# Performance work log

Measured on AMD Instinct MI355X. Metric: run time of the kernel, lower is better.

The kernel has to match this reference:

```python
import jax, jax.numpy as jnp
import numpy as np

B, T, C, H = 8, 2048, 1024, 64

def setup_inputs() -> dict:
    key = jax.random.key(0)
    k0, k1, k2, k3 = jax.random.split(key, 4)
    s = C ** -0.5
    return {
        "x": jax.random.normal(k0, (B, T, C), dtype=jnp.float32),
        "Wq": jax.random.normal(k1, (C, H), dtype=jnp.float32) * s,
        "Wk": jax.random.normal(k2, (C, H), dtype=jnp.float32) * s,
        "Wv": jax.random.normal(k3, (C, H), dtype=jnp.float32) * s,
    }

def reference(x, Wq, Wk, Wv):
    # x: [B,T,C]; Wq/Wk/Wv: [C,H]
    q = jnp.einsum('btc,ch->bth', x, Wq)
    k = jnp.einsum('btc,ch->bth', x, Wk)
    v = jnp.einsum('btc,ch->bth', x, Wv)
    Tn, Cn = x.shape[1], x.shape[2]
    # NOTE: original scales by C**-0.5 (n_embed), not head_size**-0.5
    wei = jnp.einsum('bqh,bkh->bqk', q, k) * (Cn ** -0.5)  # [B,T,T]
    causal = jnp.tril(jnp.ones((Tn, Tn), dtype=bool))
    wei = jnp.where(causal, wei, -jnp.inf)
    wei = jax.nn.softmax(wei, axis=-1)
    # dropout is identity in eval mode
    out = jnp.einsum('bqk,bkh->bqh', wei, v)  # [B,T,H]
    return out
```

## Files before the change

### kernel.cpp

```cpp
#include <hip/hip_runtime.h>
#include <hip/hip_bf16.h>

typedef __attribute__((ext_vector_type(8))) short short8;
typedef __attribute__((ext_vector_type(4))) float f32x4;
typedef __attribute__((ext_vector_type(4))) unsigned short u16x4;
typedef unsigned short u16;

#define Bn 8
#define Tn 2048
#define Cn 1024
#define Hn 64
#define Mrows (Bn * Tn)

__device__ __forceinline__ u16 bfu(float f) {
    __hip_bfloat16 h = __float2bfloat16(f);
    union { __hip_bfloat16 h; u16 u; } c; c.h = h; return c.u;
}

__device__ __forceinline__ short8 cvt8(f32x4 a0, f32x4 a1) {
    short8 r;
    r[0] = (short)bfu(a0[0]); r[1] = (short)bfu(a0[1]);
    r[2] = (short)bfu(a0[2]); r[3] = (short)bfu(a0[3]);
    r[4] = (short)bfu(a1[0]); r[5] = (short)bfu(a1[1]);
    r[6] = (short)bfu(a1[2]); r[7] = (short)bfu(a1[3]);
    return r;
}

__global__ void convert_w3(const float* __restrict__ Wq, const float* __restrict__ Wk,
                           const float* __restrict__ Wv, u16* __restrict__ wtf, float qscale) {
    int widx = blockIdx.x * 256 + threadIdx.x;
    int mat = widx >> 16;
    int rem = widx & 65535;
    int k = rem >> 6, n = rem & 63;
    const float* W = mat == 0 ? Wq : (mat == 1 ? Wk : Wv);
    float s = mat == 0 ? qscale : 1.0f;
    int ct = mat * 4 + (n >> 4);
    int lane = ((k >> 3) & 3) * 16 + (n & 15);
    wtf[(size_t)(ct * 32 + (k >> 5)) * 512 + lane * 8 + (k & 7)] = bfu(W[rem] * s);
}

__global__ __launch_bounds__(512) void qkv_proj(const float* __restrict__ x,
                                                const u16* __restrict__ wtf,
                                                u16* __restrict__ qfl,
                                                u16* __restrict__ kfl,
                                                u16* __restrict__ vfl) {
    __shared__ u16 As[2][32][136];
    const int tid = threadIdx.x;
    const int lane = tid & 63;
    const int wid = tid >> 6;
    const int wm = wid >> 2;
    const int wn = wid & 3;
    const int l15 = lane & 15;
    const int lhi = lane >> 4;
    const int row0 = blockIdx.x * 32;

    const int arow = tid >> 4;
    const int ac0 = (tid & 15) * 8;
    const float* asrc = x + (size_t)(row0 + arow) * Cn + ac0;

    f32x4 acc[3];
    for (int nj = 0; nj < 3; ++nj) acc[nj] = f32x4{0.f, 0.f, 0.f, 0.f};

    f32x4 r0 = *(const f32x4*)(asrc);
    f32x4 r1 = *(const f32x4*)(asrc + 4);
    *(short8*)&As[0][arow][ac0] = cvt8(r0, r1);
    r0 = *(const f32x4*)(asrc + 128);
    r1 = *(const f32x4*)(asrc + 132);
    __syncthreads();

    for (int ks = 0; ks < 8; ++ks) {
        const int cur = ks & 1;
        if (ks < 7) {
            *(short8*)&As[cur ^ 1][arow][ac0] = cvt8(r0, r1);
            if (ks < 6) {
                const float* nsrc = asrc + (size_t)(ks + 2) * 128;
                r0 = *(const f32x4*)(nsrc);
                r1 = *(const f32x4*)(nsrc + 4);
            }
        }
        #pragma unroll
        for (int kc = 0; kc < 4; ++kc) {
            short8 af = *(const short8*)&As[cur][wm * 16 + l15][kc * 32 + lhi * 8];
            #pragma unroll
            for (int nj = 0; nj < 3; ++nj) {
                short8 bf = *(const short8*)(wtf + (size_t)((wn * 3 + nj) * 32 + ks * 4 + kc) * 512 + lane * 8);
                acc[nj] = __builtin_amdgcn_mfma_f32_16x16x32_bf16(af, bf, acc[nj], 0, 0, 0);
            }
        }
        __syncthreads();
    }

    const int growb = row0 + wm * 16 + lhi * 4;
    const int bI = growb >> 11;
    const int tloc = growb & 2047;
    #pragma unroll
    for (int nj = 0; nj < 3; ++nj) {
        const int gcolb = wn * 48 + nj * 16;
        const int matid = gcolb >> 6;
        const int d0 = gcolb & 63;
        if (matid < 2) {
            u16* dst = matid == 0 ? qfl : kfl;
            const int g = tloc >> 4;
            const int lhid = ((d0 & 31) + l15) >> 3;
            const size_t base = ((size_t)(bI * 128 + g) * 2 + (d0 >> 5)) * 512
                                + (size_t)lhid * 128 + (l15 & 7);
            for (int r = 0; r < 4; ++r)
                dst[base + (size_t)(lhi * 4 + r) * 8] = bfu(acc[nj][r]);
        } else {
            const int kt64 = tloc >> 6;
            const int tin = tloc & 63;
            const int kcv = tin >> 5;
            const int lhiv = (tin & 31) >> 3;
            const int e0 = tin & 7;
            const int dt = d0 >> 4;
            u16x4 pk;
            pk[0] = bfu(acc[nj][0]); pk[1] = bfu(acc[nj][1]);
            pk[2] = bfu(acc[nj][2]); pk[3] = bfu(acc[nj][3]);
            *(u16x4*)(vfl + ((size_t)((bI * 32 + kt64) * 4 + dt) * 2 + kcv) * 512
                          + (size_t)(lhiv * 16 + l15) * 8 + e0) = pk;
        }
    }
}

__global__ __launch_bounds__(256) void attn_fwd(const u16* __restrict__ qfl,
                                                const u16* __restrict__ kfl,
                                                const u16* __restrict__ vfl,
                                                float* __restrict__ out) {
    __shared__ float o_lds[4][16][68];
    __shared__ float ml_lds[4][2][16];
    __shared__ u16 pl[4][16][72];
    const int tid = threadIdx.x;
    const int lane = tid & 63;
    const int w = tid >> 6;
    const int l15 = lane & 15, lhi = lane >> 4;
    const int idx = (int)blockIdx.x;
    const int qt = 127 - (idx >> 3);
    const int b = idx & 7;
    const int nkt = (qt >> 2) + 1;
    const int q0 = qt * 16;

    const u16* qb = qfl + (size_t)b * 131072;
    const u16* kb = kfl + (size_t)b * 131072;
    const u16* vb = vfl + (size_t)b * 131072;

    short8 qf[2];
    #pragma unroll
    for (int kc = 0; kc < 2; ++kc)
        qf[kc] = *(const short8*)(qb + ((size_t)(qt * 2 + kc) * 64 + lane) * 8);

    float m = -1e30f, lpart = 0.f;
    f32x4 o[4];
    for (int dt = 0; dt < 4; ++dt) o[dt] = f32x4{0.f, 0.f, 0.f, 0.f};

    for (int kbi = w; kbi < nkt; kbi += 4) {
        const int k0 = kbi * 64;
        short8 kf[2][4], vf[4][2];
        #pragma unroll
        for (int kc = 0; kc < 2; ++kc)
            #pragma unroll
            for (int kt = 0; kt < 4; ++kt)
                kf[kc][kt] = *(const short8*)(kb + ((size_t)((kbi * 4 + kt) * 2 + kc) * 64 + lane) * 8);
        #pragma unroll
        for (int dt = 0; dt < 4; ++dt)
            #pragma unroll
            for (int kc = 0; kc < 2; ++kc)
                vf[dt][kc] = *(const short8*)(vb + ((size_t)((kbi * 4 + dt) * 2 + kc) * 512 + lane * 8));

        f32x4 sacc[4];
        for (int kt = 0; kt < 4; ++kt) sacc[kt] = f32x4{0.f, 0.f, 0.f, 0.f};
        #pragma unroll
        for (int kc = 0; kc < 2; ++kc)
            #pragma unroll
            for (int kt = 0; kt < 4; ++kt)
                sacc[kt] = __builtin_amdgcn_mfma_f32_16x16x32_bf16(kf[kc][kt], qf[kc], sacc[kt], 0, 0, 0);

        if (kbi == nkt - 1) {
            for (int kt = 0; kt < 4; ++kt)
                for (int r = 0; r < 4; ++r) {
                    int kg = k0 + kt * 16 + lhi * 4 + r;
                    if (kg > q0 + l15) sacc[kt][r] = -3.0e38f;
                }
        }
        f32x4 mx0, mx1;
        for (int e = 0; e < 4; ++e) {
            mx0[e] = fmaxf(sacc[0][e], sacc[1][e]);
            mx1[e] = fmaxf(sacc[2][e], sacc[3][e]);
        }
        float tmax = -3.0e38f;
        for (int e = 0; e < 4; ++e) tmax = fmaxf(tmax, fmaxf(mx0[e], mx1[e]));
        tmax = fmaxf(tmax, __shfl_xor(tmax, 16));
        tmax = fmaxf(tmax, __shfl_xor(tmax, 32));
        if (!__all(tmax <= m + 8.0f)) {
            float mnew = fmaxf(m, tmax);
            float corr = exp2f(m - mnew);
            m = mnew;
            lpart *= corr;
            for (int r = 0; r < 4; ++r) {
                float cr = __shfl(corr, lhi * 4 + r);
                for (int dt = 0; dt < 4; ++dt) o[dt][r] *= cr;
            }
        }
        float psum = 0.f;
        for (int kt = 0; kt < 4; ++kt)
            for (int r = 0; r < 4; ++r) {
                float p = exp2f(sacc[kt][r] - m);
                sacc[kt][r] = p;
                psum += p;
            }
        lpart += psum;
        for (int kt = 0; kt < 4; ++kt) {
            u16x4 pk;
            pk[0] = bfu(sacc[kt][0]); pk[1] = bfu(sacc[kt][1]);
            pk[2] = bfu(sacc[kt][2]); pk[3] = bfu(sacc[kt][3]);
            *(u16x4*)&pl[w][l15][kt * 16 + lhi * 4] = pk;
        }
        short8 pf[2];
        #pragma unroll
        for (int kc = 0; kc < 2; ++kc)
            pf[kc] = *(const short8*)&pl[w][l15][kc * 32 + lhi * 8];
        #pragma unroll
        for (int dt = 0; dt < 4; ++dt)
            #pragma unroll
            for (int kc = 0; kc < 2; ++kc)
                o[dt] = __builtin_amdgcn_mfma_f32_16x16x32_bf16(pf[kc], vf[dt][kc], o[dt], 0, 0, 0);
    }
    float lsum = lpart;
    lsum += __shfl_xor(lsum, 16);
    lsum += __shfl_xor(lsum, 32);

    for (int dt = 0; dt < 4; ++dt)
        for (int r = 0; r < 4; ++r)
            o_lds[w][lhi * 4 + r][dt * 16 + l15] = o[dt][r];
    if (lhi == 0) {
        ml_lds[w][0][l15] = m;
        ml_lds[w][1][l15] = lsum;
    }
    __syncthreads();

    float* ob = out + ((size_t)b * Tn + q0) * Hn;
    #pragma unroll
    for (int i = 0; i < 4; ++i) {
        const int e = tid + 256 * i;
        const int row = e >> 6, d = e & 63;
        float M = -3.0e38f;
        #pragma unroll
        for (int ww = 0; ww < 4; ++ww) M = fmaxf(M, ml_lds[ww][0][row]);
        float L = 0.f, acc = 0.f;
        #pragma unroll
        for (int ww = 0; ww < 4; ++ww) {
            float wgt = exp2f(ml_lds[ww][0][row] - M);
            L += ml_lds[ww][1][row] * wgt;
            acc += o_lds[ww][row][d] * wgt;
        }
        ob[(size_t)row * Hn + d] = acc / L;
    }
}

extern "C" void kernel_launch(void* const* d_in, const int* in_sizes, int n_in,
                              void* d_out, int out_size, void* d_ws, size_t ws_size,
                              hipStream_t stream) {
    const float* x = (const float*)d_in[0];
    const float* Wq = (const float*)d_in[1];
    const float* Wk = (const float*)d_in[2];
    const float* Wv = (const float*)d_in[3];
    float* out = (float*)d_out;
    char* ws = (char*)d_ws;

    u16* wtf = (u16*)ws;
    u16* qfl = (u16*)(ws + 196608 * 2);
    u16* kfl = qfl + (size_t)Bn * 131072;
    u16* vfl = kfl + (size_t)Bn * 131072;

    const float qscale = 0.04508422002778011f;
    convert_w3<<<768, 256, 0, stream>>>(Wq, Wk, Wv, wtf, qscale);
    qkv_proj<<<Mrows / 32, 512, 0, stream>>>(x, wtf, qfl, kfl, vfl);
    attn_fwd<<<1024, 256, 0, stream>>>(qfl, kfl, vfl, out);
}
```

Before: 47.65 us.

## Fuse weight convert, QKV projection and attention into one cooperative persistent kernel

Merges the three kernels into one templated kernel and launches it cooperatively with grid-wide syncs between phases, so two kernel launch gaps go away. Blocks loop persistently over tiles and share one LDS union across phases. The projection is retiled to 256 threads per 32-row tile, with each wave computing two M subtiles, and the A-tile double buffering is dropped in favour of a single buffer with two barriers per k-step. If the cooperative launch fails it falls back to three separate launches. Risks are grid-sync cost, lower occupancy, and the attention phase's causal load imbalance now being spread over fewer resident blocks.

Result: slower. 189.1 us (+296.9%).

```diff
diff --git a/kernel.cpp b/kernel.cpp
--- a/kernel.cpp
+++ b/kernel.cpp
@@ -1,5 +1,8 @@
 #include <hip/hip_runtime.h>
 #include <hip/hip_bf16.h>
+#include <hip/hip_cooperative_groups.h>
+
+namespace cg = cooperative_groups;
 
 typedef __attribute__((ext_vector_type(8))) short short8;
 typedef __attribute__((ext_vector_type(4))) float f32x4;
@@ -26,233 +29,244 @@
     return r;
 }
 
-__global__ void convert_w3(const float* __restrict__ Wq, const float* __restrict__ Wk,
-                           const float* __restrict__ Wv, u16* __restrict__ wtf, float qscale) {
-    int widx = blockIdx.x * 256 + threadIdx.x;
-    int mat = widx >> 16;
-    int rem = widx & 65535;
-    int k = rem >> 6, n = rem & 63;
-    const float* W = mat == 0 ? Wq : (mat == 1 ? Wk : Wv);
-    float s = mat == 0 ? qscale : 1.0f;
-    int ct = mat * 4 + (n >> 4);
-    int lane = ((k >> 3) & 3) * 16 + (n & 15);
-    wtf[(size_t)(ct * 32 + (k >> 5)) * 512 + lane * 8 + (k & 7)] = bfu(W[rem] * s);
-}
-
-__global__ __launch_bounds__(512) void qkv_proj(const float* __restrict__ x,
-                                                const u16* __restrict__ wtf,
+template <int PHASE>
+__global__ __launch_bounds__(256, 4) void fused(const float* __restrict__ x,
+                                                const float* __restrict__ Wq,
+                                                const float* __restrict__ Wk,
+                                                const float* __restrict__ Wv,
+                                                u16* __restrict__ wtf,
                                                 u16* __restrict__ qfl,
                                                 u16* __restrict__ kfl,
-                                                u16* __restrict__ vfl) {
-    __shared__ u16 As[2][32][136];
+                                                u16* __restrict__ vfl,
+                                                float* __restrict__ out,
+                                                float qscale) {
+    union Smem {
+        struct { u16 As[32][136]; } q;
+        struct { float o[4][16][68]; float ml[4][2][16]; u16 pl[4][16][72]; } a;
+    };
+    __shared__ Smem sm;
     const int tid = threadIdx.x;
+    const int nb = (int)gridDim.x;
     const int lane = tid & 63;
-    const int wid = tid >> 6;
-    const int wm = wid >> 2;
-    const int wn = wid & 3;
     const int l15 = lane & 15;
     const int lhi = lane >> 4;
-    const int row0 = blockIdx.x * 32;
-
-    const int arow = tid >> 4;
-    const int ac0 = (tid & 15) * 8;
-    const float* asrc = x + (size_t)(row0 + arow) * Cn + ac0;
-
-    f32x4 acc[3];
-    for (int nj = 0; nj < 3; ++nj) acc[nj] = f32x4{0.f, 0.f, 0.f, 0.f};
-
-    f32x4 r0 = *(const f32x4*)(asrc);
-    f32x4 r1 = *(const f32x4*)(asrc + 4);
-    *(short8*)&As[0][arow][ac0] = cvt8(r0, r1);
-    r0 = *(const f32x4*)(asrc + 128);
-    r1 = *(const f32x4*)(asrc + 132);
-    __syncthreads();
-
-    for (int ks = 0; ks < 8; ++ks) {
-        const int cur = ks & 1;
-        if (ks < 7) {
-            *(short8*)&As[cur ^ 1][arow][ac0] = cvt8(r0, r1);
-            if (ks < 6) {
-                const float* nsrc = asrc + (size_t)(ks + 2) * 128;
-                r0 = *(const f32x4*)(nsrc);
-                r1 = *(const f32x4*)(nsrc + 4);
-            }
+
+    if (PHASE == -1 || PHASE == 0) {
+        for (int widx = (int)blockIdx.x * 256 + tid; widx < 196608; widx += nb * 256) {
+            int mat = widx >> 16;
+            int rem = widx & 65535;
+            int k = rem >> 6, n = rem & 63;
+            const float* W = mat == 0 ? Wq : (mat == 1 ? Wk : Wv);
+            float s = mat == 0 ? qscale : 1.0f;
+            int ct = mat * 4 + (n >> 4);
+            int ln = ((k >> 3) & 3) * 16 + (n & 15);
+            wtf[(size_t)(ct * 32 + (k >> 5)) * 512 + ln * 8 + (k & 7)] = bfu(W[rem] * s);
         }
-        #pragma unroll
-        for (int kc = 0; kc < 4; ++kc) {
-            short8 af = *(const short8*)&As[cur][wm * 16 + l15][kc * 32 + lhi * 8];
-            #pragma unroll
-            for (int nj = 0; nj < 3; ++nj) {
-                short8 bf = *(const short8*)(wtf + (size_t)((wn * 3 + nj) * 32 + ks * 4 + kc) * 512 + lane * 8);
-                acc[nj] = __builtin_amdgcn_mfma_f32_16x16x32_bf16(af, bf, acc[nj], 0, 0, 0);
+    }
+    if (PHASE == -1) cg::this_grid().sync();
+
+    if (PHASE == -1 || PHASE == 1) {
+        const int wn = tid >> 6;
+        const int arow = tid >> 3;
+        const int ac0 = (tid & 7) * 16;
+        for (int tile = (int)blockIdx.x; tile < 512; tile += nb) {
+            const int row0 = tile * 32;
+            const float* asrc = x + (size_t)(row0 + arow) * Cn + ac0;
+
+            f32x4 acc[2][3];
+            for (int mt = 0; mt < 2; ++mt)
+                for (int nj = 0; nj < 3; ++nj) acc[mt][nj] = f32x4{0.f, 0.f, 0.f, 0.f};
+
+            f32x4 ra0 = *(const f32x4*)(asrc);
+            f32x4 ra1 = *(const f32x4*)(asrc + 4);
+            f32x4 ra2 = *(const f32x4*)(asrc + 8);
+            f32x4 ra3 = *(const f32x4*)(asrc + 12);
+
+            for (int ks = 0; ks < 8; ++ks) {
+                __syncthreads();
+                *(short8*)&sm.q.As[arow][ac0]     = cvt8(ra0, ra1);
+                *(short8*)&sm.q.As[arow][ac0 + 8] = cvt8(ra2, ra3);
+                __syncthreads();
+                #pragma unroll
+                for (int kc = 0; kc < 4; ++kc) {
+                    short8 af0 = *(const short8*)&sm.q.As[l15][kc * 32 + lhi * 8];
+                    short8 af1 = *(const short8*)&sm.q.As[16 + l15][kc * 32 + lhi * 8];
+                    #pragma unroll
+                    for (int nj = 0; nj < 3; ++nj) {
+                        short8 bf = *(const short8*)(wtf + (size_t)((wn * 3 + nj) * 32 + ks * 4 + kc) * 512 + lane * 8);
+                        acc[0][nj] = __builtin_amdgcn_mfma_f32_16x16x32_bf16(af0, bf, acc[0][nj], 0, 0, 0);
+                        acc[1][nj] = __builtin_amdgcn_mfma_f32_16x16x32_bf16(af1, bf, acc[1][nj], 0, 0, 0);
+                    }
+                }
+                if (ks < 7) {
+                    const float* nsrc = asrc + (size_t)(ks + 1) * 128;
+                    ra0 = *(const f32x4*)(nsrc);
+                    ra1 = *(const f32x4*)(nsrc + 4);
+                    ra2 = *(const f32x4*)(nsrc + 8);
+                    ra3 = *(const f32x4*)(nsrc + 12);
+                }
+            }
+
+            for (int mt = 0; mt < 2; ++mt) {
+                const int growb = row0 + mt * 16 + lhi * 4;
+                const int bI = growb >> 11;
+                const int tloc = growb & 2047;
+                for (int nj = 0; nj < 3; ++nj) {
+                    const int gcolb = wn * 48 + nj * 16;
+                    const int matid = gcolb >> 6;
+                    const int d0 = gcolb & 63;
+                    if (matid < 2) {
+                        u16* dst = matid == 0 ? qfl : kfl;
+                        const int g = tloc >> 4;
+                        const int lhid = ((d0 & 31) + l15) >> 3;
+                        const size_t base = ((size_t)(bI * 128 + g) * 2 + (d0 >> 5)) * 512
+                                            + (size_t)lhid * 128 + (l15 & 7);
+                        for (int r = 0; r < 4; ++r)
+                            dst[base + (size_t)(lhi * 4 + r) * 8] = bfu(acc[mt][nj][r]);
+                    } else {
+                        const int kt64 = tloc >> 6;
+                        const int tin = tloc & 63;
+                        const int kcv = tin >> 5;
+                        const int lhiv = (tin & 31) >> 3;
+                        const int e0 = tin & 7;
+                        const int dt = d0 >> 4;
+                        u16x4 pk;
+                        pk[0] = bfu(acc[mt][nj][0]); pk[1] = bfu(acc[mt][nj][1]);
+                        pk[2] = bfu(acc[mt][nj][2]); pk[3] = bfu(acc[mt][nj][3]);
+                        *(u16x4*)(vfl + ((size_t)((bI * 32 + kt64) * 4 + dt) * 2 + kcv) * 512
+                                      + (size_t)(lhiv * 16 + l15) * 8 + e0) = pk;
+                    }
+                }
             }
         }
-        __syncthreads();
-    }
-
-    const int growb = row0 + wm * 16 + lhi * 4;
-    const int bI = growb >> 11;
-    const int tloc = growb & 2047;
-    #pragma unroll
-    for (int nj = 0; nj < 3; ++nj) {
-        const int gcolb = wn * 48 + nj * 16;
-        const int matid = gcolb >> 6;
-        const int d0 = gcolb & 63;
-        if (matid < 2) {
-            u16* dst = matid == 0 ? qfl : kfl;
-            const int g = tloc >> 4;
-            const int lhid = ((d0 & 31) + l15) >> 3;
-            const size_t base = ((size_t)(bI * 128 + g) * 2 + (d0 >> 5)) * 512
-                                + (size_t)lhid * 128 + (l15 & 7);
-            for (int r = 0; r < 4; ++r)
-                dst[base + (size_t)(lhi * 4 + r) * 8] = bfu(acc[nj][r]);
-        } else {
-            const int kt64 = tloc >> 6;
-            const int tin = tloc & 63;
-            const int kcv = tin >> 5;
-            const int lhiv = (tin & 31) >> 3;
-            const int e0 = tin & 7;
-            const int dt = d0 >> 4;
-            u16x4 pk;
-            pk[0] = bfu(acc[nj][0]); pk[1] = bfu(acc[nj][1]);
-            pk[2] = bfu(acc[nj][2]); pk[3] = bfu(acc[nj][3]);
-            *(u16x4*)(vfl + ((size_t)((bI * 32 + kt64) * 4 + dt) * 2 + kcv) * 512
-                          + (size_t)(lhiv * 16 + l15) * 8 + e0) = pk;
-        }
-    }
-}
-
-__global__ __launch_bounds__(256) void attn_fwd(const u16* __restrict__ qfl,
-                                                const u16* __restrict__ kfl,
-                                                const u16* __restrict__ vfl,
-                                                float* __restrict__ out) {
-    __shared__ float o_lds[4][16][68];
-    __shared__ float ml_lds[4][2][16];
-    __shared__ u16 pl[4][16][72];
-    const int tid = threadIdx.x;
-    const int lane = tid & 63;
-    const int w = tid >> 6;
-    const int l15 = lane & 15, lhi = lane >> 4;
-    const int idx = (int)blockIdx.x;
-    const int qt = 127 - (idx >> 3);
-    const int b = idx & 7;
-    const int nkt = (qt >> 2) + 1;
-    const int q0 = qt * 16;
-
-    const u16* qb = qfl + (size_t)b * 131072;
-    const u16* kb = kfl + (size_t)b * 131072;
-    const u16* vb = vfl + (size_t)b * 131072;
-
-    short8 qf[2];
-    #pragma unroll
-    for (int kc = 0; kc < 2; ++kc)
-        qf[kc] = *(const short8*)(qb + ((size_t)(qt * 2 + kc) * 64 + lane) * 8);
-
-    float m = -1e30f, lpart = 0.f;
-    f32x4 o[4];
-    for (int dt = 0; dt < 4; ++dt) o[dt] = f32x4{0.f, 0.f, 0.f, 0.f};
-
-    for (int kbi = w; kbi < nkt; kbi += 4) {
-        const int k0 = kbi * 64;
-        short8 kf[2][4], vf[4][2];
-        #pragma unroll
-        for (int kc = 0; kc < 2; ++kc)
-            #pragma unroll
-            for (int kt = 0; kt < 4; ++kt)
-                kf[kc][kt] = *(const short8*)(kb + ((size_t)((kbi * 4 + kt) * 2 + kc) * 64 + lane) * 8);
-        #pragma unroll
-        for (int dt = 0; dt < 4; ++dt)
+    }
+    if (PHASE == -1) cg::this_grid().sync();
+
+    if (PHASE == -1 || PHASE == 2) {
+        const int w = tid >> 6;
+        for (int unit = (int)blockIdx.x; unit < 1024; unit += nb) {
+            const int qt = 127 - (unit >> 3);
+            const int b = unit & 7;
+            const int nkt = (qt >> 2) + 1;
+            const int q0 = qt * 16;
+
+            const u16* qb = qfl + (size_t)b * 131072;
+            const u16* kb = kfl + (size_t)b * 131072;
+            const u16* vb = vfl + (size_t)b * 131072;
+
+            short8 qf[2];
             #pragma unroll
             for (int kc = 0; kc < 2; ++kc)
-                vf[dt][kc] = *(const short8*)(vb + ((size_t)((kbi * 4 + dt) * 2 + kc) * 512 + lane * 8));
-
-        f32x4 sacc[4];
-        for (int kt = 0; kt < 4; ++kt) sacc[kt] = f32x4{0.f, 0.f, 0.f, 0.f};
-        #pragma unroll
-        for (int kc = 0; kc < 2; ++kc)
+                qf[kc] = *(const short8*)(qb + ((size_t)(qt * 2 + kc) * 64 + lane) * 8);
+
+            float m = -1e30f, lpart = 0.f;
+            f32x4 o[4];
+            for (int dt = 0; dt < 4; ++dt) o[dt] = f32x4{0.f, 0.f, 0.f, 0.f};
+
+            for (int kbi = w; kbi < nkt; kbi += 4) {
+                const int k0 = kbi * 64;
+                short8 kf[2][4], vf[4][2];
+                #pragma unroll
+                for (int kc = 0; kc < 2; ++kc)
+                    #pragma unroll
+                    for (int kt = 0; kt < 4; ++kt)
+                        kf[kc][kt] = *(const short8*)(kb + ((size_t)((kbi * 4 + kt) * 2 + kc) * 64 + lane) * 8);
+                #pragma unroll
+                for (int dt = 0; dt < 4; ++dt)
+                    #pragma unroll
+                    for (int kc = 0; kc < 2; ++kc)
+                        vf[dt][kc] = *(const short8*)(vb + ((size_t)((kbi * 4 + dt) * 2 + kc) * 512 + lane * 8));
+
+                f32x4 sacc[4];
+                for (int kt = 0; kt < 4; ++kt) sacc[kt] = f32x4{0.f, 0.f, 0.f, 0.f};
+                #pragma unroll
+                for (int kc = 0; kc < 2; ++kc)
+                    #pragma unroll
+                    for (int kt = 0; kt < 4; ++kt)
+                        sacc[kt] = __builtin_amdgcn_mfma_f32_16x16x32_bf16(kf[kc][kt], qf[kc], sacc[kt], 0, 0, 0);
+
+                if (kbi == nkt - 1) {
+                    for (int kt = 0; kt < 4; ++kt)
+                        for (int r = 0; r < 4; ++r) {
+                            int kg = k0 + kt * 16 + lhi * 4 + r;
+                            if (kg > q0 + l15) sacc[kt][r] = -3.0e38f;
+                        }
+                }
+                f32x4 mx0, mx1;
+                for (int e = 0; e < 4; ++e) {
+                    mx0[e] = fmaxf(sacc[0][e], sacc[1][e]);
+                    mx1[e] = fmaxf(sacc[2][e], sacc[3][e]);
+                }
+                float tmax = -3.0e38f;
+                for (int e = 0; e < 4; ++e) tmax = fmaxf(tmax, fmaxf(mx0[e], mx1[e]));
+                tmax = fmaxf(tmax, __shfl_xor(tmax, 16));
+                tmax = fmaxf(tmax, __shfl_xor(tmax, 32));
+                if (!__all(tmax <= m + 8.0f)) {
+                    float mnew = fmaxf(m, tmax);
+                    float corr = exp2f(m - mnew);
+                    m = mnew;
+                    lpart *= corr;
+                    for (int r = 0; r < 4; ++r) {
+                        float cr = __shfl(corr, lhi * 4 + r);
+                        for (int dt = 0; dt < 4; ++dt) o[dt][r] *= cr;
+                    }
+                }
+                float psum = 0.f;
+                for (int kt = 0; kt < 4; ++kt)
+                    for (int r = 0; r < 4; ++r) {
+                        float p = exp2f(sacc[kt][r] - m);
+                        sacc[kt][r] = p;
+                        psum += p;
+                    }
+                lpart += psum;
+                for (int kt = 0; kt < 4; ++kt) {
+                    u16x4 pk;
+                    pk[0] = bfu(sacc[kt][0]); pk[1] = bfu(sacc[kt][1]);
+                    pk[2] = bfu(sacc[kt][2]); pk[3] = bfu(sacc[kt][3]);
+                    *(u16x4*)&sm.a.pl[w][l15][kt * 16 + lhi * 4] = pk;
+                }
+                short8 pf[2];
+                #pragma unroll
+                for (int kc = 0; kc < 2; ++kc)
+                    pf[kc] = *(const short8*)&sm.a.pl[w][l15][kc * 32 + lhi * 8];
+                #pragma unroll
+                for (int dt = 0; dt < 4; ++dt)
+                    #pragma unroll
+                    for (int kc = 0; kc < 2; ++kc)
+                        o[dt] = __builtin_amdgcn_mfma_f32_16x16x32_bf16(pf[kc], vf[dt][kc], o[dt], 0, 0, 0);
+            }
+            float lsum = lpart;
+            lsum += __shfl_xor(lsum, 16);
+            lsum += __shfl_xor(lsum, 32);
+
+            for (int dt = 0; dt < 4; ++dt)
+                for (int r = 0; r < 4; ++r)
+                    sm.a.o[w][lhi * 4 + r][dt * 16 + l15] = o[dt][r];
+            if (lhi == 0) {
+                sm.a.ml[w][0][l15] = m;
+                sm.a.ml[w][1][l15] = lsum;
+            }
+            __syncthreads();
+
+            float* ob = out + ((size_t)b * Tn + q0) * Hn;
             #pragma unroll
-            for (int kt = 0; kt < 4; ++kt)
-                sacc[kt] = __builtin_amdgcn_mfma_f32_16x16x32_bf16(kf[kc][kt], qf[kc], sacc[kt], 0, 0, 0);
-
-        if (kbi == nkt - 1) {
-            for (int kt = 0; kt < 4; ++kt)
-                for (int r = 0; r < 4; ++r) {
-                    int kg = k0 + kt * 16 + lhi * 4 + r;
-                    if (kg > q0 + l15) sacc[kt][r] = -3.0e38f;
-                }
+            for (int i = 0; i < 4; ++i) {
+                const int e = tid + 256 * i;
+                const int row = e >> 6, d = e & 63;
+                float M = -3.0e38f;
+                #pragma unroll
+                for (int ww = 0; ww < 4; ++ww) M = fmaxf(M, sm.a.ml[ww][0][row]);
+                float L = 0.f, acc = 0.f;
+                #pragma unroll
+                for (int ww = 0; ww < 4; ++ww) {
+                    float wgt = exp2f(sm.a.ml[ww][0][row] - M);
+                    L += sm.a.ml[ww][1][row] * wgt;
+                    acc += sm.a.o[ww][row][d] * wgt;
+                }
+                ob[(size_t)row * Hn + d] = acc / L;
+            }
+            __syncthreads();
         }
-        f32x4 mx0, mx1;
-        for (int e = 0; e < 4; ++e) {
-            mx0[e] = fmaxf(sacc[0][e], sacc[1][e]);
-            mx1[e] = fmaxf(sacc[2][e], sacc[3][e]);
-        }
-        float tmax = -3.0e38f;
-        for (int e = 0; e < 4; ++e) tmax = fmaxf(tmax, fmaxf(mx0[e], mx1[e]));
-        tmax = fmaxf(tmax, __shfl_xor(tmax, 16));
-        tmax = fmaxf(tmax, __shfl_xor(tmax, 32));
-        if (!__all(tmax <= m + 8.0f)) {
-            float mnew = fmaxf(m, tmax);
-            float corr = exp2f(m - mnew);
-            m = mnew;
-            lpart *= corr;
-            for (int r = 0; r < 4; ++r) {
-                float cr = __shfl(corr, lhi * 4 + r);
-                for (int dt = 0; dt < 4; ++dt) o[dt][r] *= cr;
-            }
-        }
-        float psum = 0.f;
-        for (int kt = 0; kt < 4; ++kt)
-            for (int r = 0; r < 4; ++r) {
-                float p = exp2f(sacc[kt][r] - m);
-                sacc[kt][r] = p;
-                psum += p;
-            }
-        lpart += psum;
-        for (int kt = 0; kt < 4; ++kt) {
-            u16x4 pk;
-            pk[0] = bfu(sacc[kt][0]); pk[1] = bfu(sacc[kt][1]);
-            pk[2] = bfu(sacc[kt][2]); pk[3] = bfu(sacc[kt][3]);
-            *(u16x4*)&pl[w][l15][kt * 16 + lhi * 4] = pk;
-        }
-        short8 pf[2];
-        #pragma unroll
-        for (int kc = 0; kc < 2; ++kc)
-            pf[kc] = *(const short8*)&pl[w][l15][kc * 32 + lhi * 8];
-        #pragma unroll
-        for (int dt = 0; dt < 4; ++dt)
-            #pragma unroll
-            for (int kc = 0; kc < 2; ++kc)
-                o[dt] = __builtin_amdgcn_mfma_f32_16x16x32_bf16(pf[kc], vf[dt][kc], o[dt], 0, 0, 0);
-    }
-    float lsum = lpart;
-    lsum += __shfl_xor(lsum, 16);
-    lsum += __shfl_xor(lsum, 32);
-
-    for (int dt = 0; dt < 4; ++dt)
-        for (int r = 0; r < 4; ++r)
-            o_lds[w][lhi * 4 + r][dt * 16 + l15] = o[dt][r];
-    if (lhi == 0) {
-        ml_lds[w][0][l15] = m;
-        ml_lds[w][1][l15] = lsum;
-    }
-    __syncthreads();
-
-    float* ob = out + ((size_t)b * Tn + q0) * Hn;
-    #pragma unroll
-    for (int i = 0; i < 4; ++i) {
-        const int e = tid + 256 * i;
-        const int row = e >> 6, d = e & 63;
-        float M = -3.0e38f;
-        #pragma unroll
-        for (int ww = 0; ww < 4; ++ww) M = fmaxf(M, ml_lds[ww][0][row]);
-        float L = 0.f, acc = 0.f;
-        #pragma unroll
-        for (int ww = 0; ww < 4; ++ww) {
-            float wgt = exp2f(ml_lds[ww][0][row] - M);
-            L += ml_lds[ww][1][row] * wgt;
-            acc += o_lds[ww][row][d] * wgt;
-        }
-        ob[(size_t)row * Hn + d] = acc / L;
     }
 }
 
@@ -270,9 +284,30 @@
     u16* qfl = (u16*)(ws + 196608 * 2);
     u16* kfl = qfl + (size_t)Bn * 131072;
     u16* vfl = kfl + (size_t)Bn * 131072;
-
-    const float qscale = 0.04508422002778011f;
-    convert_w3<<<768, 256, 0, stream>>>(Wq, Wk, Wv, wtf, qscale);
-    qkv_proj<<<Mrows / 32, 512, 0, stream>>>(x, wtf, qfl, kfl, vfl);
-    attn_fwd<<<1024, 256, 0, stream>>>(qfl, kfl, vfl, out);
+    float qscale = 0.04508422002778011f;
+
+    int dev = 0;
+    (void)hipGetDevice(&dev);
+    int cus = 0;
+    if (hipDeviceGetAttribute(&cus, hipDeviceAttributeMultiprocessorCount, dev) != hipSuccess || cus <= 0)
+        cus = 256;
+    int nbpm = 0;
+    hipError_t qe = hipOccupancyMaxActiveBlocksPerMultiprocessor(
+        &nbpm, reinterpret_cast<const void*>(fused<-1>), 256, 0);
+    int grid = (qe == hipSuccess && nbpm > 0) ? nbpm * cus : 0;
+    if (grid > 1024) grid = 1024;
+
+    hipError_t le = hipErrorUnknown;
+    if (grid >= 64) {
+        void* args[] = {(void*)&x, (void*)&Wq, (void*)&Wk, (void*)&Wv,
+                        (void*)&wtf, (void*)&qfl, (void*)&kfl, (void*)&vfl,
+                        (void*)&out, (void*)&qscale};
+        le = hipLaunchCooperativeKernel(reinterpret_cast<const void*>(fused<-1>),
+                                        dim3(grid), dim3(256), args, 0, stream);
+    }
+    if (le != hipSuccess) {
+        fused<0><<<768, 256, 0, stream>>>(x, Wq, Wk, Wv, wtf, qfl, kfl, vfl, out, qscale);
+        fused<1><<<512, 256, 0, stream>>>(x, Wq, Wk, Wv, wtf, qfl, kfl, vfl, out, qscale);
+        fused<2><<<1024, 256, 0, stream>>>(x, Wq, Wk, Wv, wtf, qfl, kfl, vfl, out, qscale);
+    }
 }
```
